# Performance work log

Hardware: AMD Instinct MI355X
Metric: run time of the kernel (lower is better)

## Reference

```python
import jax, jax.numpy as jnp
import numpy as np
from jax import lax

K = 3      # kernel_size
C = 64     # n_feat
B, H, W = 2, 256, 256


def _conv(x, w, b, pad):
    # NCHW conv, stride 1
    out = lax.conv_general_dilated(x, w, (1, 1), [(pad, pad), (pad, pad)],
                                   dimension_numbers=('NCHW', 'OIHW', 'NCHW'))
    return out + b[None, :, None, None]


def _prelu(x, a):
    # nn.PReLU() with a single shared learnable slope (init 0.25)
    return jnp.where(x >= 0, x, a * x)


def setup_inputs():
    key = jax.random.key(0)
    ks = jax.random.split(key, 20)
    s = 0.05
    def w(k, shape):
        return jax.random.normal(k, shape, jnp.float32) * s
    inp = {
        'image': jax.random.normal(ks[0], (B, C, H, W), jnp.float32),
        'guidance': jax.random.normal(ks[1], (B, C, H, W), jnp.float32),
        # self.tensor: 1x1 conv (2C -> C) + PReLU (shared with jbf_conv's act)
        'tensor_w': w(ks[2], (C, 2 * C, 1, 1)),
        'tensor_b': jnp.zeros((C,), jnp.float32),
        'a_jbf': jnp.full((1,), 0.25, jnp.float32),
        'kg_w1': w(ks[3], (C, C, 3, 3)), 'kg_b1': jnp.zeros((C,), jnp.float32),
        'kg_w2': w(ks[4], (C, C, 3, 3)), 'kg_b2': jnp.zeros((C,), jnp.float32),
        'kg_w3': w(ks[5], (C, C, 3, 3)), 'kg_b3': jnp.zeros((C,), jnp.float32),
        'kg_w4': w(ks[6], (C, C, 3, 3)), 'kg_b4': jnp.zeros((C,), jnp.float32),
        'kg_w5': w(ks[7], (K * K * C, C, 1, 1)),
        'kg_b5': jnp.zeros((K * K * C,), jnp.float32),
        'a_kg': jnp.full((1,), 0.25, jnp.float32),
        # jbf_conv: 3x3 C->C, PReLU (shared a_jbf), 3x3 C->C
        'jbf_w1': w(ks[8], (C, C, 3, 3)), 'jbf_b1': jnp.zeros((C,), jnp.float32),
        'jbf_w2': w(ks[9], (C, C, 3, 3)), 'jbf_b2': jnp.zeros((C,), jnp.float32),
    }
    return inp


def reference(image, guidance, tensor_w, tensor_b, a_jbf,
              kg_w1, kg_b1, kg_w2, kg_b2, kg_w3, kg_b3, kg_w4, kg_b4,
              kg_w5, kg_b5, a_kg, jbf_w1, jbf_b1, jbf_w2, jbf_b2):
    b, c, h, w = image.shape
    # fuse target+guidance features
    t = _prelu(_conv(jnp.concatenate([image, guidance], axis=1), tensor_w, tensor_b, 0), a_jbf)
    # concat_kg: predict per-pixel dynamic kernel (b, K*K*c, h, w)
    y = t
    for wt, bs in ((kg_w1, kg_b1), (kg_w2, kg_b2), (kg_w3, kg_b3), (kg_w4, kg_b4)):
        y = _prelu(_conv(y, wt, bs, 1), a_kg)
    bi_kernel = _conv(y, kg_w5, kg_b5, 0)
    # unfold: torch layout is channel-major (c, ki, kj) along dim 1
    p = (K - 1) // 2
    xp = jnp.pad(image, ((0, 0), (0, 0), (p, p), (p, p)))
    taps = [xp[:, :, i:i + h, j:j + w] for i in range(K) for j in range(K)]
    patch = jnp.stack(taps, axis=2).reshape(b, c * K * K, h, w)
    # NOTE: faithful to source -- (c*K*K) flat layout reinterpreted as (K*K, c)
    jbf = (patch * bi_kernel).reshape(b, K * K, c, h, w).sum(axis=1)
    out = _conv(_prelu(_conv(jbf, jbf_w1, jbf_b1, 1), a_jbf), jbf_w2, jbf_b2, 1)
    return out + image
```

## Files before the change

kernel.cpp:

```cpp
#include <hip/hip_runtime.h>

#define HW 65536

typedef __bf16 bf16x8 __attribute__((ext_vector_type(8)));
typedef float f32x16 __attribute__((ext_vector_type(16)));

__device__ inline unsigned short f2bf(float x) {
    union { float f; unsigned u; } v; v.f = x;
    unsigned r = v.u + 0x7FFF + ((v.u >> 16) & 1);
    return (unsigned short)(r >> 16);
}
__device__ inline unsigned pk2(float a, float b) {
    unsigned r;
    asm("v_cvt_pk_bf16_f32 %0, %1, %2" : "=v"(r) : "v"(a), "v"(b));
    return r;
}
__device__ inline float bfhi2f(unsigned u) {
    union { unsigned u; float f; } v; v.u = u & 0xffff0000u; return v.f;
}
__device__ inline float bflo2f(unsigned u) {
    union { unsigned u; float f; } v; v.u = u << 16; return v.f;
}

union FragU { uint4 u; bf16x8 v; };
__device__ inline bf16x8 ld_frag(const uint4* p) { FragU t; t.u = *p; return t.v; }


__global__ __launch_bounds__(256) void k_pre(
    const float* __restrict__ img, const float* __restrict__ gd,
    const float* __restrict__ w0, const float* __restrict__ w1,
    const float* __restrict__ w2, const float* __restrict__ w3,
    const float* __restrict__ w4, const float* __restrict__ w5,
    const float* __restrict__ w5c, const float* __restrict__ tw,
    unsigned short* __restrict__ imgT, unsigned short* __restrict__ gdT,
    unsigned short* __restrict__ wT)
{
    __shared__ float sT[64 * 66];
    int tid = threadIdx.x;
    int y = blockIdx.y;
    if (y < 4) {
        int z = y;
        int b = z & 1;
        const float* src = (z >> 1) ? gd : img;
        unsigned short* dst = (z >> 1) ? gdT : imgT;
        int px0 = blockIdx.x * 64;
        size_t sbase = (size_t)b * 64 * HW + px0;

#pragma unroll
        for (int i = 0; i < 4; ++i) {
            int e = i * 256 + tid;
            int ic = e >> 4, seg = e & 15;
            float4 v = *(const float4*)(src + sbase + (size_t)ic * HW + seg * 4);
            float* p = &sT[ic * 66 + seg * 4];
            ((float2*)p)[0] = make_float2(v.x, v.y);
            ((float2*)p)[1] = make_float2(v.z, v.w);
        }
        __syncthreads();

        size_t dbase = (size_t)b * HW * 64 + (size_t)px0 * 64;
#pragma unroll
        for (int k = 0; k < 2; ++k) {
            int idx = k * 256 + tid;
            int px = idx >> 3, u = idx & 7;
            union { uint4 q; unsigned w[4]; } ou;
#pragma unroll
            for (int j = 0; j < 4; ++j)
                ou.w[j] = pk2(sT[(u * 8 + 2 * j) * 66 + px],
                              sT[(u * 8 + 2 * j + 1) * 66 + px]);
            *(uint4*)(dst + dbase + (size_t)px * 64 + u * 8) = ou.q;
        }
    } else {
        const float* ws_[6] = {w0, w1, w2, w3, w4, w5};
        for (int e = blockIdx.x * 256 + tid; e < 266240; e += 262144) {
            if (e < 221184) {
                int y2 = e / 36864, e2 = e - y2 * 36864;
                int tap = e2 >> 12, oc = (e2 >> 6) & 63, ic = e2 & 63;
                int igg = ic >> 3, j = ic & 7;
                int dst = ((tap * 8 + igg) * 64 + oc) * 8 + j;
                wT[(size_t)y2 * 36864 + dst] = f2bf(ws_[y2][(oc * 64 + ic) * 9 + tap]);
            } else if (e < 258048) {
                int e2 = e - 221184;
                wT[(size_t)6 * 36864 + e2] = f2bf(w5c[e2]);
            } else {
                int e2 = e - 258048;
                int oc = e2 >> 7, ic = e2 & 127;
                int kg = ic >> 3, j = ic & 7;
                wT[(size_t)7 * 36864 + ((kg * 64 + oc) << 3) + j] = f2bf(tw[e2]);
            }
        }
    }
}

__global__ __launch_bounds__(256, 3) void k_fuse3(
    const unsigned short* __restrict__ imgT, const unsigned short* __restrict__ gdT,
    const unsigned short* __restrict__ wTf,
    const unsigned short* __restrict__ w1T, const unsigned short* __restrict__ w2T,
    const float* __restrict__ tb, const float* __restrict__ b1,
    const float* __restrict__ b2, const float* __restrict__ ajbf,
    const float* __restrict__ akg, unsigned short* __restrict__ out)
{
    __shared__ __align__(16) char smem[53760];
    uint4* sS0 = (uint4*)smem;
    uint4* sS1 = (uint4*)(smem + 19200);

    int tid = threadIdx.x;
    int wv = tid >> 6, lane = tid & 63;
    int half = lane >> 5, l31 = lane & 31;
    int w2 = wv >> 1, g = wv & 1;
    int lin = blockIdx.x + (blockIdx.y << 4) + (blockIdx.z << 9);
    int slab = lin & 7, sub = lin >> 3;
    int b = slab >> 2;
    int y0 = (slab & 3) * 64 + (sub >> 4) * 8;
    int x0 = (sub & 15) * 16;
    const size_t zbase = (size_t)b * HW * 64;
    const uint4* wgf = (const uint4*)wTf;
    const uint4* wg1 = (const uint4*)w1T;
    const uint4* wg2 = (const uint4*)w2T;

    float rT[16], rB1[16], rB2[16];
#pragma unroll
    for (int q2 = 0; q2 < 4; ++q2)
#pragma unroll
        for (int j = 0; j < 4; ++j) {
            int oc = w2 * 32 + j + 8 * q2 + 4 * half;
            rT[q2 * 4 + j]  = tb[oc];
            rB1[q2 * 4 + j] = b1[oc];
            rB2[q2 * 4 + j] = b2[oc];
        }

    auto loadS = [&](int t, int h, uint4* rx) {
        const unsigned short* src = t ? gdT : imgT;
#pragma unroll
        for (int i = 0; i < 4; ++i) {
            int e = i * 256 + tid;
            int cell = e >> 2, ig = e & 3;
            int r = cell / 20, c2 = cell - r * 20;
            int gy = y0 - 2 + r, gx = x0 - 2 + c2;
            rx[i] = make_uint4(0, 0, 0, 0);
            if (e < 960 && gy >= 0 && gy < 256 && gx >= 0 && gx < 256)
                rx[i] = *(const uint4*)(src + zbase + ((size_t)(gy * 256 + gx)) * 64 + h * 32 + ig * 8);
        }
    };
    auto writeS = [&](uint4* s, const uint4* rx) {
#pragma unroll
        for (int i = 0; i < 4; ++i) {
            int e = i * 256 + tid;
            if (e < 960) s[(e >> 2) * 5 + (e & 3)] = rx[i];
        }
    };

    int cell0[4];
#pragma unroll
    for (int s = 0; s < 4; ++s) {
        int c = g * 128 + s * 32 + l31;
        cell0[s] = c < 240 ? c : 239;
    }
    f32x16 acc0[4];
#pragma unroll
    for (int s = 0; s < 4; ++s)
#pragma unroll
        for (int r = 0; r < 16; ++r) acc0[s][r] = 0.f;

    auto mm1 = [&](int t, int h, const uint4* sS) {
        __builtin_amdgcn_s_setprio(1);
#pragma unroll
        for (int c = 0; c < 2; ++c) {
            int ig = c * 2 + half;
            int kg = t * 8 + h * 4 + ig;
            bf16x8 af = ld_frag(&wgf[kg * 64 + w2 * 32 + l31]);
#pragma unroll
            for (int s = 0; s < 4; ++s) {
                bf16x8 bb = ld_frag(&sS[cell0[s] * 5 + ig]);
                acc0[s] = __builtin_amdgcn_mfma_f32_32x32x16_bf16(af, bb, acc0[s], 0, 0, 0);
            }
        }
        __builtin_amdgcn_s_setprio(0);
    };

    uint4 rx[4];
    loadS(0, 0, rx);
    writeS(sS0, rx);
    loadS(0, 1, rx);
    __syncthreads();
    mm1(0, 0, sS0);
    writeS(sS1, rx);
    loadS(1, 0, rx);
    __syncthreads();
    mm1(0, 1, sS1);
    writeS(sS0, rx);
    loadS(1, 1, rx);
    __syncthreads();
    mm1(1, 0, sS0);
    writeS(sS1, rx);
    __syncthreads();
    mm1(1, 1, sS1);

    float s_jbf = ajbf[0], s_kg = akg[0];
    __syncthreads();
    unsigned short* sC0 = (unsigned short*)smem;
#pragma unroll
    for (int s = 0; s < 4; ++s) {
        int cell = g * 128 + s * 32 + l31;
        if (cell < 240) {
            int R = cell / 20, C = cell - R * 20;
            int gy = y0 - 2 + R, gx = x0 - 2 + C;
            bool inb = (gy >= 0 && gy < 256 && gx >= 0 && gx < 256);
#pragma unroll
            for (int q2 = 0; q2 < 4; ++q2) {
                float vv[4];
#pragma unroll
                for (int j = 0; j < 4; ++j) {
                    int r = (q2 << 2) | j;
                    float v = acc0[s][r] + rT[q2 * 4 + j];
                    v = (v >= 0.f) ? v : s_jbf * v;
                    vv[j] = inb ? v : 0.f;
                }
                int up = (w2 * 4 + q2) ^ (cell & 7);
                *(uint2*)&sC0[cell * 64 + up * 8 + half * 4] =
                    make_uint2(pk2(vv[0], vv[1]), pk2(vv[2], vv[3]));
            }
        }
    }
    __syncthreads();

    int cellv[3], ibv[3];
#pragma unroll
    for (int s = 0; s < 3; ++s) {
        int c = g * 96 + s * 32 + l31;
        cellv[s] = c;
        int cc = c < 180 ? c : 179;
        ibv[s] = (cc / 18) * 20 + (cc % 18);
    }
    f32x16 acc1[3];
#pragma unroll
    for (int s = 0; s < 3; ++s)
#pragma unroll
        for (int r = 0; r < 16; ++r) acc1[s][r] = 0.f;

    {
        const uint4* sC04 = (const uint4*)smem;
        __builtin_amdgcn_s_setprio(1);
#pragma unroll
        for (int dy = 0; dy < 3; ++dy) {
#pragma unroll
            for (int dx = 0; dx < 3; ++dx) {
                int tap = dy * 3 + dx;
                int doff = dy * 20 + dx;
#pragma unroll
                for (int c4 = 0; c4 < 4; ++c4) {
                    int unit = c4 * 2 + half;
                    bf16x8 af = ld_frag(&wg1[(tap * 8 + unit) * 64 + w2 * 32 + l31]);
#pragma unroll
                    for (int s = 0; s < 3; ++s) {
                        int cc = ibv[s] + doff;
                        bf16x8 bb = ld_frag(&sC04[cc * 8 + (unit ^ (cc & 7))]);
                        acc1[s] = __builtin_amdgcn_mfma_f32_32x32x16_bf16(af, bb, acc1[s], 0, 0, 0);
                    }
                }
            }
        }
        __builtin_amdgcn_s_setprio(0);
    }

    unsigned short* sC1 = (unsigned short*)(smem + 30720);
#pragma unroll
    for (int s = 0; s < 3; ++s) {
        int cell = cellv[s];
        if (cell < 180) {
            int orow = cell / 18, ocol = cell - orow * 18;
            int gy = y0 - 1 + orow, gx = x0 - 1 + ocol;
            bool inb = (gy >= 0 && gy < 256 && gx >= 0 && gx < 256);
#pragma unroll
            for (int q2 = 0; q2 < 4; ++q2) {
                float vv[4];
#pragma unroll
                for (int j = 0; j < 4; ++j) {
                    int r = (q2 << 2) | j;
                    float v = acc1[s][r] + rB1[q2 * 4 + j];
                    v = (v >= 0.f) ? v : s_kg * v;
                    vv[j] = inb ? v : 0.f;
                }
                int up = (w2 * 4 + q2) ^ (cell & 7);
                *(uint2*)&sC1[cell * 64 + up * 8 + half * 4] =
                    make_uint2(pk2(vv[0], vv[1]), pk2(vv[2], vv[3]));
            }
        }
    }
    __syncthreads();

    f32x16 acc2[2];
#pragma unroll
    for (int s = 0; s < 2; ++s)
#pragma unroll
        for (int r = 0; r < 16; ++r) acc2[s][r] = 0.f;

    int rowS[2], colS[2];
#pragma unroll
    for (int s = 0; s < 2; ++s) {
        int px = g * 64 + s * 32 + l31;
        rowS[s] = px >> 4; colS[s] = px & 15;
    }
    {
        const uint4* sC14 = (const uint4*)(smem + 30720);
        __builtin_amdgcn_s_setprio(1);
#pragma unroll
        for (int dy = 0; dy < 3; ++dy) {
#pragma unroll
            for (int dx = 0; dx < 3; ++dx) {
                int tap = dy * 3 + dx;
#pragma unroll
                for (int c = 0; c < 4; ++c) {
                    int ig = c * 2 + half;
                    bf16x8 af = ld_frag(&wg2[(tap * 8 + ig) * 64 + w2 * 32 + l31]);
#pragma unroll
                    for (int s = 0; s < 2; ++s) {
                        int cl = (rowS[s] + dy) * 18 + colS[s] + dx;
                        bf16x8 bb = ld_frag(&sC14[cl * 8 + (ig ^ (cl & 7))]);
                        acc2[s] = __builtin_amdgcn_mfma_f32_32x32x16_bf16(af, bb, acc2[s], 0, 0, 0);
                    }
                }
            }
        }
        __builtin_amdgcn_s_setprio(0);
    }

    unsigned short* sT16 = (unsigned short*)smem;
#pragma unroll
    for (int s = 0; s < 2; ++s) {
        int px = g * 64 + s * 32 + l31;
#pragma unroll
        for (int q2 = 0; q2 < 4; ++q2) {
            float vv[4];
#pragma unroll
            for (int j = 0; j < 4; ++j) {
                int r = (q2 << 2) | j;
                float v = acc2[s][r] + rB2[q2 * 4 + j];
                vv[j] = (v >= 0.f) ? v : s_kg * v;
            }
            int up = (w2 * 4 + q2) ^ (px & 7);
            uint2* p = (uint2*)&sT16[px * 64 + up * 8 + half * 4];
            *p = make_uint2(pk2(vv[0], vv[1]), pk2(vv[2], vv[3]));
        }
    }
    __syncthreads();
#pragma unroll
    for (int k = 0; k < 4; ++k) {
        int idx = k * 256 + tid;
        int row = idx >> 7, rem = idx & 127;
        int col = rem >> 3, u = rem & 7;
        int px = row * 16 + col;
        uint4 v = *(uint4*)&sT16[px * 64 + (u ^ (px & 7)) * 8];
        *(uint4*)(out + zbase + ((size_t)((y0 + row) * 256 + x0 + col)) * 64 + u * 8) = v;
    }
}

#define XU 5

template<int MODE>
__global__ __launch_bounds__(256, 4) void k_conv2x(
    const unsigned short* __restrict__ in,
    const unsigned short* __restrict__ w1T, const unsigned short* __restrict__ w2T,
    const float* __restrict__ b1, const float* __restrict__ b2,
    const float* __restrict__ a, const float* __restrict__ res,
    void* __restrict__ outv)
{
    __shared__ __align__(16) char smem[38912];
    uint4* sIn0 = (uint4*)smem;
    uint4* sIn1 = (uint4*)(smem + 19200);
    float* sB = (float*)(smem + 38400);

    int tid = threadIdx.x;
    int wv = tid >> 6, lane = tid & 63;
    int half = lane >> 5, l31 = lane & 31;
    int w2 = wv >> 1, g = wv & 1;
    int lin = blockIdx.x + (blockIdx.y << 4) + (blockIdx.z << 9);
    int slab = lin & 7, sub = lin >> 3;
    int b = slab >> 2;
    int y0 = (slab & 3) * 64 + (sub >> 4) * 8;
    int x0 = (sub & 15) * 16;
    const size_t zbase = (size_t)b * HW * 64;
    const uint4* wg1 = (const uint4*)w1T;
    const uint4* wg2 = (const uint4*)w2T;

    if (tid < 64) sB[tid] = b1[tid];
    else if (tid < 128) sB[tid] = b2[tid - 64];

    auto loadIn = [&](int h, uint4* rx) {
#pragma unroll
        for (int i = 0; i < 4; ++i) {
            int e = i * 256 + tid;
            int cell = e >> 2, ig = e & 3;
            int r = cell / 20, c2 = cell - r * 20;
            int gy = y0 - 2 + r, gx = x0 - 2 + c2;
            rx[i] = make_uint4(0, 0, 0, 0);
            bool act = (i < 3) || (e < 960);
            if (act && gy >= 0 && gy < 256 && gx >= 0 && gx < 256)
                rx[i] = *(const uint4*)(in + zbase + ((size_t)(gy * 256 + gx)) * 64 + h * 32 + ig * 8);
        }
    };
    auto writeIn = [&](uint4* s, const uint4* rx) {
#pragma unroll
        for (int i = 0; i < 4; ++i) {
            int e = i * 256 + tid;
            if (i < 3 || e < 960) s[(e >> 2) * XU + (e & 3)] = rx[i];
        }
    };

    int cellv[3], ibv[3];
#pragma unroll
    for (int s = 0; s < 3; ++s) {
        int c = g * 96 + s * 32 + l31;
        cellv[s] = c;
        int cc = c < 180 ? c : 179;
        ibv[s] = (cc / 18) * 20 + (cc % 18);
    }

    f32x16 acc1[3];
#pragma unroll
    for (int s = 0; s < 3; ++s)
#pragma unroll
        for (int r = 0; r < 16; ++r) acc1[s][r] = 0.f;

    auto conv1_h = [&](int h, const uint4* sInp) {
        __builtin_amdgcn_s_setprio(1);
#pragma unroll
        for (int dy = 0; dy < 3; ++dy) {
#pragma unroll
            for (int dx = 0; dx < 3; ++dx) {
                int tap = dy * 3 + dx;
                int doff = dy * 20 + dx;
#pragma unroll
                for (int c = 0; c < 2; ++c) {
                    int ig = c * 2 + half;
                    bf16x8 af = ld_frag(&wg1[(tap * 8 + h * 4 + ig) * 64 + w2 * 32 + l31]);
#pragma unroll
                    for (int s = 0; s < 3; ++s) {
                        bf16x8 bb = ld_frag(&sInp[(ibv[s] + doff) * XU + ig]);
                        acc1[s] = __builtin_amdgcn_mfma_f32_32x32x16_bf16(af, bb, acc1[s], 0, 0, 0);
                    }
                }
            }
        }
        __builtin_amdgcn_s_setprio(0);
    };

    uint4 rx[4];
    loadIn(0, rx);
    writeIn(sIn0, rx);
    uint4 ry[4];
    loadIn(1, ry);
    __syncthreads();
    conv1_h(0, sIn0);
    writeIn(sIn1, ry);
    __syncthreads();
    conv1_h(1, sIn1);

    float s1 = a[0];
    __syncthreads();
    unsigned short* sC16 = (unsigned short*)smem;
#pragma unroll
    for (int s = 0; s < 3; ++s) {
        int cell = cellv[s];
        if (cell < 180) {
            int orow = cell / 18, ocol = cell - orow * 18;
            int gy = y0 - 1 + orow, gx = x0 - 1 + ocol;
            bool inb = (gy >= 0 && gy < 256 && gx >= 0 && gx < 256);
#pragma unroll
            for (int q2 = 0; q2 < 4; ++q2) {
                float vv[4];
#pragma unroll
                for (int j = 0; j < 4; ++j) {
                    int r = (q2 << 2) | j;
                    int oc = w2 * 32 + j + 8 * q2 + 4 * half;
                    float v = acc1[s][r] + sB[oc];
                    v = (v >= 0.f) ? v : s1 * v;
                    vv[j] = inb ? v : 0.f;
                }
                int up = (w2 * 4 + q2) ^ (cell & 7);
                *(uint2*)&sC16[cell * 64 + up * 8 + half * 4] =
                    make_uint2(pk2(vv[0], vv[1]), pk2(vv[2], vv[3]));
            }
        }
    }
    __syncthreads();

    f32x16 acc2[2];
#pragma unroll
    for (int s = 0; s < 2; ++s)
#pragma unroll
        for (int r = 0; r < 16; ++r) acc2[s][r] = 0.f;

    int rowS[2], colS[2];
#pragma unroll
    for (int s = 0; s < 2; ++s) {
        int px = g * 64 + s * 32 + l31;
        rowS[s] = px >> 4; colS[s] = px & 15;
    }
    {
        const uint4* sC4 = (const uint4*)smem;
        __builtin_amdgcn_s_setprio(1);
#pragma unroll
        for (int dy = 0; dy < 3; ++dy) {
#pragma unroll
            for (int dx = 0; dx < 3; ++dx) {
                int tap = dy * 3 + dx;
#pragma unroll
                for (int c = 0; c < 4; ++c) {
                    int ig = c * 2 + half;
                    bf16x8 af = ld_frag(&wg2[(tap * 8 + ig) * 64 + w2 * 32 + l31]);
#pragma unroll
                    for (int s = 0; s < 2; ++s) {
                        int cl = (rowS[s] + dy) * 18 + colS[s] + dx;
                        bf16x8 bb = ld_frag(&sC4[cl * 8 + (ig ^ (cl & 7))]);
                        acc2[s] = __builtin_amdgcn_mfma_f32_32x32x16_bf16(af, bb, acc2[s], 0, 0, 0);
                    }
                }
            }
        }
        __builtin_amdgcn_s_setprio(0);
    }

    if (MODE == 0) {
        __syncthreads();
        unsigned short* sT16 = (unsigned short*)smem;
#pragma unroll
        for (int s = 0; s < 2; ++s) {
            int px = g * 64 + s * 32 + l31;
#pragma unroll
            for (int q2 = 0; q2 < 4; ++q2) {
                float vv[4];
#pragma unroll
                for (int j = 0; j < 4; ++j) {
                    int r = (q2 << 2) | j;
                    int oc = w2 * 32 + j + 8 * q2 + 4 * half;
                    float v = acc2[s][r] + sB[64 + oc];
                    vv[j] = (v >= 0.f) ? v : s1 * v;
                }
                int up = (w2 * 4 + q2) ^ (px & 7);
                uint2* p = (uint2*)&sT16[px * 64 + up * 8 + half * 4];
                *p = make_uint2(pk2(vv[0], vv[1]), pk2(vv[2], vv[3]));
            }
        }
        __syncthreads();
        unsigned short* outT = (unsigned short*)outv;
#pragma unroll
        for (int k = 0; k < 4; ++k) {
            int idx = k * 256 + tid;
            int row = idx >> 7, rem = idx & 127;
            int col = rem >> 3, u = rem & 7;
            int px = row * 16 + col;
            uint4 v = *(uint4*)&sT16[px * 64 + (u ^ (px & 7)) * 8];
            *(uint4*)(outT + zbase + ((size_t)((y0 + row) * 256 + x0 + col)) * 64 + u * 8) = v;
        }
    } else {
        float* outF = (float*)outv;
#pragma unroll
        for (int s = 0; s < 2; ++s) {
            int px = g * 64 + s * 32 + l31;
            int y = y0 + (px >> 4), x = x0 + (px & 15);
            size_t pbase = (size_t)b * 64 * HW + (size_t)y * 256 + x;
#pragma unroll
            for (int r = 0; r < 16; ++r) {
                int oc = w2 * 32 + (r & 3) + 8 * (r >> 2) + 4 * half;
                float v = acc2[s][r] + sB[64 + oc];
                v += res[pbase + (size_t)oc * HW];
                outF[pbase + (size_t)oc * HW] = v;
            }
        }
    }
}

struct OffTab { unsigned v[9][32]; int chlo[9]; };
constexpr OffTab make_tab() {
    OffTab t{};
    for (int kk = 0; kk < 9; ++kk) {
        int chlo = (kk * 64) / 9;
        t.chlo[kk] = chlo;
        for (int ot = 0; ot < 2; ++ot)
            for (int r = 0; r < 16; ++r) {
                int cc0 = ot * 32 + (r & 3) + 8 * (r >> 2);
                int q0 = kk * 64 + cc0, q1 = q0 + 4;
                int o0 = (q0 / 9 - chlo) * 360 + (q0 % 9 / 3) * 40 + (q0 % 9 % 3);
                int o1 = (q1 / 9 - chlo) * 360 + (q1 % 9 / 3) * 40 + (q1 % 9 % 3);
                t.v[kk][ot * 16 + r] = (unsigned)o0 | ((unsigned)o1 << 16);
            }
    }
    return t;
}
__constant__ OffTab kOff = make_tab();

__global__ __launch_bounds__(256, 2) void k_jbfm5(
    const unsigned short* __restrict__ in, const float* __restrict__ img,
    const unsigned short* __restrict__ w1T, const unsigned short* __restrict__ w2T,
    const unsigned short* __restrict__ w5T,
    const float* __restrict__ b1, const float* __restrict__ b2,
    const float* __restrict__ b5, const float* __restrict__ akg,
    unsigned short* __restrict__ out)
{
    __shared__ __align__(16) char smem[80896];
    float* sB = (float*)(smem + 80384);
    uint4* sIn0 = (uint4*)smem;
    uint4* sIn1 = (uint4*)(smem + 34560);
    uint4* sY = (uint4*)(smem + 43520);
    float* sB5 = (float*)(smem + 39424);
    unsigned short* sT16 = (unsigned short*)smem;

    int tid = threadIdx.x;
    int wv = tid >> 6, lane = tid & 63;
    int half = lane >> 5, l31 = lane & 31;
    int w2 = wv >> 1, g = wv & 1;
    int lin = blockIdx.x + (blockIdx.y << 3) + (blockIdx.z << 8);
    int slab = lin & 7, sub = lin >> 3;
    int b = slab >> 2;
    int y0 = (slab & 3) * 64 + (sub >> 3) * 8;
    int x0 = (sub & 7) * 32;
    size_t zbase = (size_t)b * HW * 64;
    size_t ibase = (size_t)b * 64 * HW;
    const uint4* wg1 = (const uint4*)w1T;
    const uint4* wg2 = (const uint4*)w2T;

    if (tid < 64) sB[tid] = b1[tid];
    else if (tid < 128) sB[tid] = b2[tid - 64];

    auto loadIn = [&](int h, uint4* rx) {
#pragma unroll
        for (int i = 0; i < 7; ++i) {
            int e = i * 256 + tid;
            int cell = e >> 2, ig = e & 3;
            int r = cell / 36, c2 = cell - r * 36;
            int gy = y0 - 2 + r, gx = x0 - 2 + c2;
            rx[i] = make_uint4(0, 0, 0, 0);
            if (e < 1728 && gy >= 0 && gy < 256 && gx >= 0 && gx < 256)
                rx[i] = *(const uint4*)(in + zbase + ((size_t)(gy * 256 + gx)) * 64 + h * 32 + ig * 8);
        }
    };
    auto writeIn = [&](uint4* s, const uint4* rx) {
#pragma unroll
        for (int i = 0; i < 7; ++i) {
            int e = i * 256 + tid;
            if (e < 1728) s[(e >> 2) * XU + (e & 3)] = rx[i];
        }
    };

    int cellv[6], ibv[6];
    bool val[6];
#pragma unroll
    for (int s = 0; s < 6; ++s) {
        int c = g * 170 + s * 32 + l31;
        val[s] = (s * 32 + l31) < 170;
        cellv[s] = c;
        int cc = c < 340 ? c : 339;
        ibv[s] = (cc / 34) * 36 + (cc % 34);
    }
    f32x16 acc1[6];
#pragma unroll
    for (int s = 0; s < 6; ++s)
#pragma unroll
        for (int r = 0; r < 16; ++r) acc1[s][r] = 0.f;

    auto conv1_h = [&](int h, const uint4* sInp) {
        __builtin_amdgcn_s_setprio(1);
#pragma unroll
        for (int dy = 0; dy < 3; ++dy) {
#pragma unroll
            for (int dx = 0; dx < 3; ++dx) {
                int tap = dy * 3 + dx;
                int doff = dy * 36 + dx;
#pragma unroll
                for (int c = 0; c < 2; ++c) {
                    int ig = c * 2 + half;
                    bf16x8 af = ld_frag(&wg1[(tap * 8 + h * 4 + ig) * 64 + w2 * 32 + l31]);
#pragma unroll
                    for (int s = 0; s < 6; ++s) {
                        bf16x8 bb = ld_frag(&sInp[(ibv[s] + doff) * XU + ig]);
                        acc1[s] = __builtin_amdgcn_mfma_f32_32x32x16_bf16(af, bb, acc1[s], 0, 0, 0);
                    }
                }
            }
        }
        __builtin_amdgcn_s_setprio(0);
    };

    uint4 rx[7], ry[7];
    loadIn(0, rx);
    writeIn(sIn0, rx);
    loadIn(1, ry);
    __syncthreads();
    conv1_h(0, sIn0);
    writeIn(sIn1, ry);
    __syncthreads();
    conv1_h(1, sIn1);

    float s_kg = akg[0];
    __syncthreads();
    unsigned short* sC16 = (unsigned short*)smem;
#pragma unroll
    for (int s = 0; s < 6; ++s) {
        if (val[s]) {
            int cell = cellv[s];
            int row = cell / 34, col = cell - row * 34;
            int gy = y0 - 1 + row, gx = x0 - 1 + col;
            bool inb = (gy >= 0 && gy < 256 && gx >= 0 && gx < 256);
#pragma unroll
            for (int q2 = 0; q2 < 4; ++q2) {
                float vv[4];
#pragma unroll
                for (int j = 0; j < 4; ++j) {
                    int r = (q2 << 2) | j;
                    int oc = w2 * 32 + j + 8 * q2 + 4 * half;
                    float v = acc1[s][r] + sB[oc];
                    v = (v >= 0.f) ? v : s_kg * v;
                    vv[j] = inb ? v : 0.f;
                }
                int up = (w2 * 4 + q2) ^ (cell & 7);
                *(uint2*)&sC16[cell * 64 + up * 8 + half * 4] =
                    make_uint2(pk2(vv[0], vv[1]), pk2(vv[2], vv[3]));
            }
        }
    }
    __syncthreads();

    f32x16 acc2[4];
#pragma unroll
    for (int s = 0; s < 4; ++s)
#pragma unroll
        for (int r = 0; r < 16; ++r) acc2[s][r] = 0.f;

    int rowS[4], colS[4];
#pragma unroll
    for (int s = 0; s < 4; ++s) {
        int p = g * 128 + s * 32 + l31;
        rowS[s] = p >> 5; colS[s] = p & 31;
    }
    {
        const uint4* sC4 = (const uint4*)smem;
        __builtin_amdgcn_s_setprio(1);
#pragma unroll
        for (int dy = 0; dy < 3; ++dy) {
#pragma unroll
            for (int dx = 0; dx < 3; ++dx) {
                int tap = dy * 3 + dx;
#pragma unroll
                for (int c = 0; c < 4; ++c) {
                    int ig = c * 2 + half;
                    bf16x8 af = ld_frag(&wg2[(tap * 8 + ig) * 64 + w2 * 32 + l31]);
#pragma unroll
                    for (int s = 0; s < 4; ++s) {
                        int cl = (rowS[s] + dy) * 34 + colS[s] + dx;
                        bf16x8 bb = ld_frag(&sC4[cl * 8 + (ig ^ (cl & 7))]);
                        acc2[s] = __builtin_amdgcn_mfma_f32_32x32x16_bf16(af, bb, acc2[s], 0, 0, 0);
                    }
                }
            }
        }
        __builtin_amdgcn_s_setprio(0);
    }

    {
        unsigned short* sY16 = (unsigned short*)(smem + 43520);
#pragma unroll
        for (int s = 0; s < 4; ++s) {
            int px = g * 128 + s * 32 + l31;
#pragma unroll
            for (int q2 = 0; q2 < 4; ++q2) {
                int ig = w2 * 4 + q2;
                float vv[4];
#pragma unroll
                for (int j = 0; j < 4; ++j) {
                    int r = (q2 << 2) | j;
                    int oc = w2 * 32 + j + 8 * q2 + 4 * half;
                    float v = acc2[s][r] + sB[64 + oc];
                    vv[j] = (v >= 0.f) ? v : s_kg * v;
                }
                *(uint2*)&sY16[px * 72 + ig * 8 + half * 4] =
                    make_uint2(pk2(vv[0], vv[1]), pk2(vv[2], vv[3]));
            }
        }
    }
    __syncthreads();

    int p_off[3], p_dst[3];
    bool p_a[3], p_b[3], p_act[3];
#pragma unroll
    for (int i = 0; i < 3; ++i) {
        int e = i * 256 + tid;
        bool act = e < 720;
        int ch = e / 90, rem = e - ch * 90;
        int rp = rem / 10, seg = rem - rp * 10;
        int gy = y0 + rp - 1;
        int gxb = x0 - 4 + seg * 4;
        bool xok = (gxb >= 0 && gxb < 256);
        p_act[i] = act;
        p_a[i] = act && xok && gy >= 0 && gy < 256;
        p_b[i] = act && xok && (gy + 1) < 256;
        p_off[i] = ch * HW + gy * 256 + gxb;
        p_dst[i] = ch * 360 + rp * 40 + seg * 4;
    }

    for (int e = tid; e < 576; e += 256) sB5[e] = b5[e];

    {
        uint4* sW50 = (uint4*)smem;
        unsigned* sP0 = (unsigned*)(smem + 16384);
#pragma unroll
        for (int u = 0; u < 2; ++u) {
            int uu = u * 256 + tid;
            int cc = uu & 63, ig = uu >> 6;
            sW50[uu] = ((const uint4*)w5T)[cc * 8 + ig];
        }
        const float* rp0 = img + ibase;
#pragma unroll
        for (int i = 0; i < 3; ++i) {
            float4 fa = make_float4(0, 0, 0, 0), fb = make_float4(0, 0, 0, 0);
            if (p_a[i]) fa = *(const float4*)(rp0 + p_off[i]);
            if (p_b[i]) fb = *(const float4*)(rp0 + p_off[i] + 256);
            if (p_act[i]) {
                uint4 pk;
                pk.x = pk2(fa.x, fb.x);
                pk.y = pk2(fa.y, fb.y);
                pk.z = pk2(fa.z, fb.z);
                pk.w = pk2(fa.w, fb.w);
                *(uint4*)&sP0[p_dst[i]] = pk;
            }
        }
    }

    float jb[2][2][16];
#pragma unroll
    for (int i = 0; i < 2; ++i)
#pragma unroll
        for (int j = 0; j < 2; ++j)
#pragma unroll
            for (int r = 0; r < 16; ++r) jb[i][j][r] = 0.f;

    __syncthreads();

#pragma unroll 1
    for (int kk = 0; kk < 9; ++kk) {
        const int cur = kk & 1;
        const uint4* sW5c = (const uint4*)(smem + cur * 8192);
        const unsigned* sPc = (const unsigned*)(smem + 16384 + cur * 11520);

        uint4 wpre0, wpre1;
        float4 pfa[3], pfb[3];
        if (kk < 8) {
            const int nk = kk + 1;
            const int chlo_n = kOff.chlo[nk];
            {
                int cc = tid & 63, ig = tid >> 6;
                wpre0 = ((const uint4*)w5T)[(nk * 64 + cc) * 8 + ig];
                int uu = 256 + tid;
                int cc1 = uu & 63, ig1 = uu >> 6;
                wpre1 = ((const uint4*)w5T)[(nk * 64 + cc1) * 8 + ig1];
            }
            const float* rp0 = img + ibase + (size_t)chlo_n * HW;
#pragma unroll
            for (int i = 0; i < 3; ++i) {
                pfa[i] = make_float4(0, 0, 0, 0);
                pfb[i] = make_float4(0, 0, 0, 0);
                if (p_a[i]) pfa[i] = *(const float4*)(rp0 + p_off[i]);
                if (p_b[i]) pfb[i] = *(const float4*)(rp0 + p_off[i] + 256);
            }
        }

        f32x16 acc[2][2];
#pragma unroll
        for (int ot = 0; ot < 2; ++ot)
#pragma unroll
            for (int r = 0; r < 16; ++r) {
                int cc0 = ot * 32 + (r & 3) + 8 * (r >> 2);
                float bv = sB5[kk * 64 + cc0 + 4 * half];
                acc[ot][0][r] = bv;
                acc[ot][1][r] = bv;
            }

        __builtin_amdgcn_s_setprio(1);
#pragma unroll
        for (int c = 0; c < 4; ++c) {
            int ig = c * 2 + half;
            bf16x8 a0 = ld_frag(&sW5c[ig * 64 + l31]);
            bf16x8 a1 = ld_frag(&sW5c[ig * 64 + 32 + l31]);
            int p0 = wv * 64 + l31;
            bf16x8 b0 = ld_frag(&sY[p0 * 9 + ig]);
            bf16x8 b1 = ld_frag(&sY[(p0 + 32) * 9 + ig]);
            acc[0][0] = __builtin_amdgcn_mfma_f32_32x32x16_bf16(a0, b0, acc[0][0], 0, 0, 0);
            acc[0][1] = __builtin_amdgcn_mfma_f32_32x32x16_bf16(a0, b1, acc[0][1], 0, 0, 0);
            acc[1][0] = __builtin_amdgcn_mfma_f32_32x32x16_bf16(a1, b0, acc[1][0], 0, 0, 0);
            acc[1][1] = __builtin_amdgcn_mfma_f32_32x32x16_bf16(a1, b1, acc[1][1], 0, 0, 0);
        }
        __builtin_amdgcn_s_setprio(0);

        {
            const unsigned* basep = sPc + wv * 80 + l31 + 3;
            const unsigned* tab = kOff.v[kk];
#pragma unroll
            for (int ot = 0; ot < 2; ++ot)
#pragma unroll
                for (int r = 0; r < 16; ++r) {
                    unsigned oo = tab[ot * 16 + r];
                    unsigned o0 = oo & 0xffffu, o1 = oo >> 16;
                    unsigned pv = basep[half ? o1 : o0];
                    jb[ot][0][r] = fmaf(acc[ot][0][r], bflo2f(pv), jb[ot][0][r]);
                    jb[ot][1][r] = fmaf(acc[ot][1][r], bfhi2f(pv), jb[ot][1][r]);
                }
        }

        if (kk < 8) {
            uint4* sW5n = (uint4*)(smem + (cur ^ 1) * 8192);
            unsigned* sPn = (unsigned*)(smem + 16384 + (cur ^ 1) * 11520);
            sW5n[tid] = wpre0;
            sW5n[256 + tid] = wpre1;
#pragma unroll
            for (int i = 0; i < 3; ++i) {
                if (p_act[i]) {
                    uint4 pk;
                    pk.x = pk2(pfa[i].x, pfb[i].x);
                    pk.y = pk2(pfa[i].y, pfb[i].y);
                    pk.z = pk2(pfa[i].z, pfb[i].z);
                    pk.w = pk2(pfa[i].w, pfb[i].w);
                    *(uint4*)&sPn[p_dst[i]] = pk;
                }
            }
        }
        __syncthreads();
    }

#pragma unroll
    for (int ot = 0; ot < 2; ++ot)
#pragma unroll
        for (int pt = 0; pt < 2; ++pt) {
            int px = wv * 64 + pt * 32 + l31;
#pragma unroll
            for (int q2 = 0; q2 < 4; ++q2) {
                int r0 = q2 << 2;
                int unit = ot * 4 + q2;
                int up = unit ^ (px & 7);
                uint2* p = (uint2*)&sT16[px * 64 + up * 8 + half * 4];
                *p = make_uint2(pk2(jb[ot][pt][r0], jb[ot][pt][r0 + 1]),
                                pk2(jb[ot][pt][r0 + 2], jb[ot][pt][r0 + 3]));
            }
        }
    __syncthreads();
#pragma unroll
    for (int k = 0; k < 8; ++k) {
        int col = tid >> 3, u = tid & 7;
        int px = k * 32 + col;
        uint4 v = *(uint4*)&sT16[px * 64 + (u ^ (px & 7)) * 8];
        *(uint4*)(out + zbase + ((size_t)((y0 + k) * 256 + x0 + col)) * 64 + u * 8) = v;
    }
}

extern "C" void kernel_launch(void* const* d_in, const int* in_sizes, int n_in,
                              void* d_out, int out_size, void* d_ws, size_t ws_size,
                              hipStream_t stream) {
    const float* img  = (const float*)d_in[0];
    const float* gd   = (const float*)d_in[1];
    const float* tw   = (const float*)d_in[2];
    const float* tb   = (const float*)d_in[3];
    const float* ajbf = (const float*)d_in[4];
    const float* kw1  = (const float*)d_in[5];
    const float* kb1  = (const float*)d_in[6];
    const float* kw2  = (const float*)d_in[7];
    const float* kb2  = (const float*)d_in[8];
    const float* kw3  = (const float*)d_in[9];
    const float* kb3  = (const float*)d_in[10];
    const float* kw4  = (const float*)d_in[11];
    const float* kb4  = (const float*)d_in[12];
    const float* kw5  = (const float*)d_in[13];
    const float* kb5  = (const float*)d_in[14];
    const float* akg  = (const float*)d_in[15];
    const float* jw1  = (const float*)d_in[16];
    const float* jb1  = (const float*)d_in[17];
    const float* jw2  = (const float*)d_in[18];
    const float* jb2  = (const float*)d_in[19];
    float* out  = (float*)d_out;

    const size_t TEN = (size_t)2 * HW * 64;
    unsigned short* bufA = (unsigned short*)d_ws;
    unsigned short* imgT = bufA + TEN;
    unsigned short* gdT  = imgT + TEN;
    unsigned short* wT   = gdT + TEN;
    unsigned short* bufC = gdT;

    dim3 gs(16, 32, 2);
    dim3 gw(8, 32, 2);

    k_pre<<<dim3(1024, 5), 256, 0, stream>>>(img, gd, kw1, kw2, kw3, kw4,
                                             jw1, jw2, kw5, tw, imgT, gdT, wT);

    k_fuse3<<<gs, 256, 0, stream>>>(imgT, gdT, wT + (size_t)7 * 36864,
                                    wT + (size_t)0 * 36864, wT + (size_t)1 * 36864,
                                    tb, kb1, kb2, ajbf, akg, bufA);

    k_jbfm5<<<gw, 256, 0, stream>>>(bufA, img,
                                    wT + (size_t)2 * 36864, wT + (size_t)3 * 36864,
                                    wT + (size_t)6 * 36864,
                                    kb3, kb4, kb5, akg, bufC);

    k_conv2x<2><<<gs, 256, 0, stream>>>(bufC, wT + (size_t)4 * 36864, wT + (size_t)5 * 36864,
                                        jb1, jb2, ajbf, img, out);
}
```

Measured before the change: 273.1 us.

## Read w5 fragments directly from global and coalesce final residual output via LDS

The 1x1 w5 weight is re-laid out in the prep kernel so MFMA A-fragments can be loaded straight from global/L2 in the jbf kernel. This drops the per-iteration LDS staging and double-buffering of w5 and shrinks the shared-memory footprint. Separately, the fp32 final output with residual add is first transposed through LDS so each thread does float4 coalesced loads and stores along x, replacing strided scalar global accesses. The cost is an extra LDS round trip and barriers in the epilogue, plus global-latency exposure for the weight loads inside the MFMA loop.

Result: no change. 276.6 us (+1.3%).

```diff
diff --git a/kernel.cpp b/kernel.cpp
--- a/kernel.cpp
+++ b/kernel.cpp
@@ -80,7 +80,10 @@
                 wT[(size_t)y2 * 36864 + dst] = f2bf(ws_[y2][(oc * 64 + ic) * 9 + tap]);
             } else if (e < 258048) {
                 int e2 = e - 221184;
-                wT[(size_t)6 * 36864 + e2] = f2bf(w5c[e2]);
+                int q = e2 >> 6, rem = e2 & 63;
+                int ig = rem >> 3, j = rem & 7;
+                int dst = (((q >> 6) * 8 + ig) * 64 + (q & 63)) * 8 + j;
+                wT[(size_t)6 * 36864 + dst] = f2bf(w5c[e2]);
             } else {
                 int e2 = e - 258048;
                 int oc = e2 >> 7, ic = e2 & 127;
@@ -553,19 +556,33 @@
             *(uint4*)(outT + zbase + ((size_t)((y0 + row) * 256 + x0 + col)) * 64 + u * 8) = v;
         }
     } else {
-        float* outF = (float*)outv;
+        __syncthreads();
+        float* sF = (float*)smem;
 #pragma unroll
         for (int s = 0; s < 2; ++s) {
             int px = g * 64 + s * 32 + l31;
-            int y = y0 + (px >> 4), x = x0 + (px & 15);
-            size_t pbase = (size_t)b * 64 * HW + (size_t)y * 256 + x;
 #pragma unroll
             for (int r = 0; r < 16; ++r) {
                 int oc = w2 * 32 + (r & 3) + 8 * (r >> 2) + 4 * half;
-                float v = acc2[s][r] + sB[64 + oc];
-                v += res[pbase + (size_t)oc * HW];
-                outF[pbase + (size_t)oc * HW] = v;
-            }
+                sF[oc * 128 + px] = acc2[s][r] + sB[64 + oc];
+            }
+        }
+        __syncthreads();
+        float* outF = (float*)outv;
+        size_t tbase = (size_t)b * 64 * HW + (size_t)y0 * 256 + x0;
+#pragma unroll
+        for (int pass = 0; pass < 8; ++pass) {
+            int item = pass * 256 + tid;
+            int seg = item & 3;
+            int chunk = item >> 2;
+            int row = chunk & 7, oc = chunk >> 3;
+            size_t ga = tbase + (size_t)oc * HW + row * 256 + seg * 4;
+            float4 rv = *(const float4*)(res + ga);
+            const float* sp = &sF[oc * 128 + row * 16 + seg * 4];
+            float4 ov;
+            ov.x = rv.x + sp[0]; ov.y = rv.y + sp[1];
+            ov.z = rv.z + sp[2]; ov.w = rv.w + sp[3];
+            *(float4*)(outF + ga) = ov;
         }
     }
 }
@@ -602,7 +619,7 @@
     uint4* sIn0 = (uint4*)smem;
     uint4* sIn1 = (uint4*)(smem + 34560);
     uint4* sY = (uint4*)(smem + 43520);
-    float* sB5 = (float*)(smem + 39424);
+    float* sB5 = (float*)(smem + 23040);
     unsigned short* sT16 = (unsigned short*)smem;
 
     int tid = threadIdx.x;
@@ -618,6 +635,7 @@
     size_t ibase = (size_t)b * 64 * HW;
     const uint4* wg1 = (const uint4*)w1T;
     const uint4* wg2 = (const uint4*)w2T;
+    const uint4* wg5 = (const uint4*)w5T;
 
     if (tid < 64) sB[tid] = b1[tid];
     else if (tid < 128) sB[tid] = b2[tid - 64];
@@ -800,14 +818,7 @@
     for (int e = tid; e < 576; e += 256) sB5[e] = b5[e];
 
     {
-        uint4* sW50 = (uint4*)smem;
-        unsigned* sP0 = (unsigned*)(smem + 16384);
-#pragma unroll
-        for (int u = 0; u < 2; ++u) {
-            int uu = u * 256 + tid;
-            int cc = uu & 63, ig = uu >> 6;
-            sW50[uu] = ((const uint4*)w5T)[cc * 8 + ig];
-        }
+        unsigned* sP0 = (unsigned*)smem;
         const float* rp0 = img + ibase;
 #pragma unroll
         for (int i = 0; i < 3; ++i) {
@@ -838,21 +849,11 @@
 #pragma unroll 1
     for (int kk = 0; kk < 9; ++kk) {
         const int cur = kk & 1;
-        const uint4* sW5c = (const uint4*)(smem + cur * 8192);
-        const unsigned* sPc = (const unsigned*)(smem + 16384 + cur * 11520);
-
-        uint4 wpre0, wpre1;
+        const unsigned* sPc = (const unsigned*)(smem + cur * 11520);
+
         float4 pfa[3], pfb[3];
         if (kk < 8) {
-            const int nk = kk + 1;
-            const int chlo_n = kOff.chlo[nk];
-            {
-                int cc = tid & 63, ig = tid >> 6;
-                wpre0 = ((const uint4*)w5T)[(nk * 64 + cc) * 8 + ig];
-                int uu = 256 + tid;
-                int cc1 = uu & 63, ig1 = uu >> 6;
-                wpre1 = ((const uint4*)w5T)[(nk * 64 + cc1) * 8 + ig1];
-            }
+            const int chlo_n = kOff.chlo[kk + 1];
             const float* rp0 = img + ibase + (size_t)chlo_n * HW;
 #pragma unroll
             for (int i = 0; i < 3; ++i) {
@@ -878,8 +879,8 @@
 #pragma unroll
         for (int c = 0; c < 4; ++c) {
             int ig = c * 2 + half;
-            bf16x8 a0 = ld_frag(&sW5c[ig * 64 + l31]);
-            bf16x8 a1 = ld_frag(&sW5c[ig * 64 + 32 + l31]);
+            bf16x8 a0 = ld_frag(&wg5[(kk * 8 + ig) * 64 + l31]);
+            bf16x8 a1 = ld_frag(&wg5[(kk * 8 + ig) * 64 + 32 + l31]);
             int p0 = wv * 64 + l31;
             bf16x8 b0 = ld_frag(&sY[p0 * 9 + ig]);
             bf16x8 b1 = ld_frag(&sY[(p0 + 32) * 9 + ig]);
@@ -906,10 +907,7 @@
         }
 
         if (kk < 8) {
-            uint4* sW5n = (uint4*)(smem + (cur ^ 1) * 8192);
-            unsigned* sPn = (unsigned*)(smem + 16384 + (cur ^ 1) * 11520);
-            sW5n[tid] = wpre0;
-            sW5n[256 + tid] = wpre1;
+            unsigned* sPn = (unsigned*)(smem + (cur ^ 1) * 11520);
 #pragma unroll
             for (int i = 0; i < 3; ++i) {
                 if (p_act[i]) {
```
